# Kernel optimization log

Hardware: AMD Instinct MI355X
Metric: run time of the kernel (lower is better)

## Reference

```python
import jax, jax.numpy as jnp
import numpy as np

# Hamilton product tables: out component q uses weight IDX[q,p] with sign SGN[q,p]
# applied to input component p. Components order: (r, i, j, k); weights order: (rr, ri, rj, rk).
IDX = np.array([[0, 1, 2, 3], [1, 0, 3, 2], [2, 3, 0, 1], [3, 2, 1, 0]])
SGN = np.array([[1., -1., -1., -1.], [1., 1., 1., -1.], [1., -1., 1., 1.], [1., 1., -1., 1.]], dtype=np.float32)


def _qlinear(x4, w, b):
    # x4: (B, 4, Cin4, H, W); w: (4, Cout4, Cin4); b: (4, Cout4)
    # Quaternion 1x1 conv == channel-mixing matmul with Hamilton sign structure.
    wstk = jnp.asarray(SGN)[:, :, None, None] * w[IDX]  # (4,4,Cout4,Cin4)
    out = jnp.einsum('qpoc,bpchw->bqohw', wstk, x4)
    return out + b[None, :, :, None, None]


def _qdwconv(x4, w, b):
    # x4: (B, 4, Cc, H, W); w: (4, Cc, 1, 3, 3) depthwise per-channel; b: (4, Cc)
    Cc = x4.shape[2]
    comps = [x4[:, p] for p in range(4)]  # each (B, Cc, H, W)
    outs = []
    for qc in range(4):
        acc = None
        for p in range(4):
            c = SGN[qc, p] * jax.lax.conv_general_dilated(
                comps[p], w[IDX[qc, p]], window_strides=(1, 1), padding='SAME',
                feature_group_count=Cc, dimension_numbers=('NCHW', 'OIHW', 'NCHW'))
            acc = c if acc is None else acc + c
        outs.append(acc + b[qc][None, :, None, None])
    return jnp.stack(outs, axis=1)  # (B, 4, Cc, H, W)


def setup_inputs() -> dict:
    key = jax.random.key(0)
    ks = jax.random.split(key, 4)
    B, Cc, H, W = 8, 256, 32, 32   # dim = 4*Cc = 1024
    dim = 4 * Cc
    num_heads, key_dim = 8, 128
    h = 3 * num_heads * key_dim    # 3072 total -> 768 per component
    x = jax.random.normal(ks[0], (B, Cc, 4, H, W), jnp.float32)
    w_qkv = jax.random.normal(ks[1], (4, h // 4, dim // 4), jnp.float32) * (1.0 / np.sqrt(dim))
    b_qkv = jnp.zeros((4, h // 4), jnp.float32)
    w_proj = jax.random.normal(ks[2], (4, dim // 4, dim // 4), jnp.float32) * (1.0 / np.sqrt(dim))
    b_proj = jnp.zeros((4, dim // 4), jnp.float32)
    w_pe = jax.random.normal(ks[3], (4, dim // 4, 1, 3, 3), jnp.float32) * (1.0 / 6.0)
    b_pe = jnp.zeros((4, dim // 4), jnp.float32)
    return {'x': x, 'w_qkv': w_qkv, 'b_qkv': b_qkv, 'w_proj': w_proj,
            'b_proj': b_proj, 'w_pe': w_pe, 'b_pe': b_pe}


def reference(x, w_qkv, b_qkv, w_proj, b_proj, w_pe, b_pe):
    B, Cc, Q, H, W = x.shape
    num_heads, key_dim = 8, 128
    scale = key_dim ** -0.5
    N = H * W
    xq = jnp.transpose(x, (0, 2, 1, 3, 4))            # (B, 4, Cc, H, W)
    qkv = _qlinear(xq, w_qkv, b_qkv)                  # (B, 4, 768, H, W)
    q4, k4, v4 = jnp.split(qkv, 3, axis=2)            # each (B, 4, 256, H, W)

    def to_heads(t):  # (B,4,Cc,H,W) -> (B, heads, key_dim, N)
        return t.reshape(B, 4 * Cc, N).reshape(B, num_heads, key_dim, N)

    q, k, v = to_heads(q4), to_heads(k4), to_heads(v4)
    scores = jnp.einsum('bhdn,bhdm->bhnm', q, k) * scale   # (B,H,N,N) fully materialized
    attn = jax.nn.softmax(scores, axis=-1)
    out = jnp.einsum('bhnm,bhdm->bhdn', attn, v)           # (B,H,key_dim,N)
    out4 = out.reshape(B, 4, Cc, H, W)
    out = _qlinear(out4, w_proj, b_proj) + _qdwconv(xq, w_pe, b_pe)
    return jnp.transpose(out, (0, 2, 1, 3, 4))             # (B, Cc, 4, H, W)
```

## Files before the change

### kernel.cpp

```cpp
#include <hip/hip_runtime.h>
#include <hip/hip_bf16.h>

typedef unsigned short u16;
typedef float f32x4 __attribute__((ext_vector_type(4)));
typedef __bf16 bf16x8 __attribute__((ext_vector_type(8)));
typedef __bf16 bf16x4 __attribute__((ext_vector_type(4)));
typedef unsigned short su8v __attribute__((ext_vector_type(8)));
typedef unsigned short su4v __attribute__((ext_vector_type(4)));
typedef short s16x4 __attribute__((ext_vector_type(4)));

#define BB 8
#define NHD 8
#define DD 128
#define NN 1024
#define DIM 1024
#define H3 3072
#define MM 8192
#define QSC (0.08838834764831845f * 1.4426950408889634f)

__constant__ int   d_IDX[16] = {0,1,2,3, 1,0,3,2, 2,3,0,1, 3,2,1,0};
__constant__ float d_SGN[16] = {1.f,-1.f,-1.f,-1.f, 1.f,1.f,1.f,-1.f,
                                1.f,-1.f,1.f,1.f,  1.f,1.f,-1.f,1.f};

__device__ __forceinline__ f32x4 mfma16(su8v a, su8v b, f32x4 c) {
  return __builtin_amdgcn_mfma_f32_16x16x32_bf16(
      __builtin_bit_cast(bf16x8, a), __builtin_bit_cast(bf16x8, b), c, 0, 0, 0);
}
__device__ __forceinline__ f32x4 mfma16h(su4v a, su4v b, f32x4 c) {
#if __has_builtin(__builtin_amdgcn_mfma_f32_16x16x16_bf16)
  return __builtin_amdgcn_mfma_f32_16x16x16_bf16(
      __builtin_bit_cast(bf16x4, a), __builtin_bit_cast(bf16x4, b), c, 0, 0, 0);
#elif __has_builtin(__builtin_amdgcn_mfma_f32_16x16x16bf16_1k)
  return __builtin_amdgcn_mfma_f32_16x16x16bf16_1k(
      __builtin_bit_cast(s16x4, a), __builtin_bit_cast(s16x4, b), c, 0, 0, 0);
#else
  f32x4 d = c;
  asm("v_mfma_f32_16x16x16_bf16 %0, %1, %2, %0" : "+v"(d) : "v"(a), "v"(b));
  return d;
#endif
}
__device__ __forceinline__ u16 f2b(float f) {
  unsigned int u = __builtin_bit_cast(unsigned int, f);
  u += 0x7fffu + ((u >> 16) & 1u);
  return (u16)(u >> 16);
}
__device__ __forceinline__ float b2f(u16 v) {
  unsigned int u = ((unsigned int)v) << 16;
  return __builtin_bit_cast(float, u);
}
typedef const __attribute__((address_space(1))) unsigned int* gas_t;
typedef __attribute__((address_space(3))) unsigned int* las_t;
__device__ __forceinline__ void gll16(const u16* g, u16* l) {
  __builtin_amdgcn_global_load_lds((gas_t)g, (las_t)l, 16, 0, 0);
}

__global__ __launch_bounds__(256) void prep_weff(
    const float* __restrict__ wqkv, const float* __restrict__ wproj,
    u16* __restrict__ weffQ, u16* __restrict__ weffP) {
  int tid = blockIdx.x * 256 + threadIdx.x;
  int stride = gridDim.x * 256;
  for (int i = tid; i < H3 * DIM; i += stride) {
    int row = i >> 10, col = i & 1023;
    int q = row / 768, o = row - q * 768;
    int p = col >> 8, c = col & 255;
    float v = d_SGN[q * 4 + p] * wqkv[(d_IDX[q * 4 + p] * 768 + o) * 256 + c];
    if (o < 256) v *= QSC;
    weffQ[i] = f2b(v);
  }
  for (int i = tid; i < DIM * DIM; i += stride) {
    int row = i >> 10, col = i & 1023;
    int q = row >> 8, o = row & 255;
    int p = col >> 8, c = col & 255;
    weffP[i] = f2b(d_SGN[q * 4 + p] * wproj[(d_IDX[q * 4 + p] * 256 + o) * 256 + c]);
  }
}

__global__ __launch_bounds__(256) void prep_x(
    const float* __restrict__ x, u16* __restrict__ Ax) {
  __shared__ u16 T[64 * 264];
  int blk = blockIdx.x;
  int nc = blk & 15;
  int cc = (blk >> 4) & 3;
  int b = blk >> 6;
  int n0 = nc * 64, c0 = cc * 64;
  int tid = threadIdx.x;
  int nseg = tid & 15, rq = tid >> 4;
#pragma unroll
  for (int pass = 0; pass < 16; ++pass) {
    int rr = pass * 16 + rq;
    int p = rr >> 6, c = rr & 63;
    float4 f = *(const float4*)(x + (((size_t)(b * 256 + c0 + c)) * 4 + p) * 1024 +
                                n0 + nseg * 4);
    T[(nseg * 4 + 0) * 264 + rr] = f2b(f.x);
    T[(nseg * 4 + 1) * 264 + rr] = f2b(f.y);
    T[(nseg * 4 + 2) * 264 + rr] = f2b(f.z);
    T[(nseg * 4 + 3) * 264 + rr] = f2b(f.w);
  }
  __syncthreads();
  int nl = tid >> 5, lc = tid & 31;
#pragma unroll
  for (int pass = 0; pass < 8; ++pass) {
    int n = pass * 8 + nl;
    su8v v = *(const su8v*)(&T[n * 264 + lc * 8]);
    int pcl = lc * 8;
    *(su8v*)(Ax + (size_t)(b * 1024 + n0 + n) * 1024 + (pcl >> 6) * 256 + c0 +
             (pcl & 63)) = v;
  }
}

template <int BM, int BN>
__device__ __forceinline__ void gemm_core8(
    const u16* __restrict__ Ag, const u16* __restrict__ Bg,
    u16* As, u16* Bs, int tid, f32x4 (&acc)[4][4]) {
  constexpr int WN = BN / 64;
  constexpr int AC = BM / 64;
  constexpr int BC = BN / 64;
  constexpr int NT = 16;
  int w = tid >> 6, lane = tid & 63, l16 = lane & 15, quad = lane >> 4;
  int wm = w / WN, wn = w % WN;
  int x7 = l16 & 7;
  int srow = lane >> 3;
  int sblk = (lane & 7) ^ srow;

  auto STAGE_A = [&](int tt, int bs) {
#pragma unroll
    for (int c = 0; c < AC; ++c) {
      int r0 = c * 64 + w * 8;
      gll16(Ag + (size_t)(r0 + srow) * 1024 + tt * 64 + sblk * 8,
            As + (size_t)bs * (BM * 64) + r0 * 64);
    }
  };
  auto STAGE_B = [&](int tt, int bs) {
#pragma unroll
    for (int c = 0; c < BC; ++c) {
      int r0 = c * 64 + w * 8;
      gll16(Bg + (size_t)(r0 + srow) * 1024 + tt * 64 + sblk * 8,
            Bs + (size_t)bs * (BN * 64) + r0 * 64);
    }
  };

  STAGE_A(0, 0); STAGE_B(0, 0);
  STAGE_A(1, 1); STAGE_B(1, 1);
  asm volatile("s_waitcnt vmcnt(6)" ::: "memory");
  __builtin_amdgcn_s_barrier();

  int cur = 0, nxt = 1, stg = 2;
  for (int t = 0; t < NT; ++t) {
    const u16* At = As + (size_t)cur * (BM * 64);
    const u16* Bt = Bs + (size_t)cur * (BN * 64);
#pragma unroll
    for (int kk = 0; kk < 2; ++kk) {
      su8v af[4], bf[4];
#pragma unroll
      for (int i = 0; i < 4; ++i)
        af[i] = *(const su8v*)(At + (wm * 64 + i * 16 + l16) * 64 +
                               ((kk * 4 + quad) ^ x7) * 8);
#pragma unroll
      for (int j = 0; j < 4; ++j)
        bf[j] = *(const su8v*)(Bt + (wn * 64 + j * 16 + l16) * 64 +
                               ((kk * 4 + quad) ^ x7) * 8);
      if (t + 2 < NT) {
        if (kk == 0) STAGE_A(t + 2, stg);
        else         STAGE_B(t + 2, stg);
      }
      __builtin_amdgcn_s_setprio(1);
#pragma unroll
      for (int i = 0; i < 4; ++i)
#pragma unroll
        for (int j = 0; j < 4; ++j)
          acc[i][j] = mfma16(af[i], bf[j], acc[i][j]);
      __builtin_amdgcn_s_setprio(0);
    }
    if (t < NT - 2)       asm volatile("s_waitcnt vmcnt(6)" ::: "memory");
    else if (t == NT - 2) asm volatile("s_waitcnt vmcnt(0)" ::: "memory");
    asm volatile("" ::: "memory");
    __builtin_amdgcn_s_barrier();
    asm volatile("" ::: "memory");
    int tmp = cur; cur = nxt; nxt = stg; stg = tmp;
  }
}

__global__ __launch_bounds__(512, 2) void gemm_qkv_mfma(
    const u16* __restrict__ Ax, const u16* __restrict__ weffQ,
    const float* __restrict__ bqkv,
    u16* __restrict__ Qb, u16* __restrict__ Kb, u16* __restrict__ VbT) {
  __shared__ u16 smem[3 * 384 * 64];
  int bn0 = blockIdx.x * 256;
  int col0 = blockIdx.y * 128;
  int q = col0 / 768;
  int off = col0 - q * 768;
  int sel = off >> 8;
  int head = (q * 256 + (off & 255)) >> 7;
  int tid = threadIdx.x;
  int w = tid >> 6, lane = tid & 63, l16 = lane & 15, quad = lane >> 4;
  f32x4 acc[4][4];
#pragma unroll
  for (int i = 0; i < 4; ++i)
#pragma unroll
    for (int j = 0; j < 4; ++j) acc[i][j] = (f32x4){0.f, 0.f, 0.f, 0.f};

  if (sel == 2) {
    gemm_core8<256, 128>(Ax + (size_t)bn0 * 1024, weffQ + (size_t)col0 * 1024,
                         smem, smem + 3 * 256 * 64, tid, acc);
    int wm = w >> 1, wn = w & 1;
#pragma unroll
    for (int j = 0; j < 4; ++j) {
      int dl = wn * 64 + j * 16 + l16;
      float bias = bqkv[col0 + dl];
      int hswap = ((dl >> 3) & 1) << 2;
#pragma unroll
      for (int i = 0; i < 4; ++i) {
        int m = bn0 + wm * 64 + i * 16 + quad * 4;
        int b = m >> 10, npos = m & 1023;
        int bh = b * NHD + head;
        su4v pk;
#pragma unroll
        for (int r = 0; r < 4; ++r) pk[r] = f2b(acc[i][j][r] + bias);
        *(su4v*)(VbT + ((size_t)bh * DD + dl) * NN + (npos ^ hswap)) = pk;
      }
    }
  } else {
    gemm_core8<128, 256>(weffQ + (size_t)col0 * 1024, Ax + (size_t)bn0 * 1024,
                         smem, smem + 3 * 128 * 64, tid, acc);
    int wm = w >> 2, wn = w & 3;
    u16* dst = (sel == 0) ? Qb : Kb;
    float sc = (sel == 0) ? (float)QSC : 1.0f;
#pragma unroll
    for (int i = 0; i < 4; ++i) {
      int dbase = wm * 64 + i * 16 + quad * 4;
      float4 b4 = *(const float4*)(bqkv + col0 + dbase);
#pragma unroll
      for (int j = 0; j < 4; ++j) {
        int n = bn0 + wn * 64 + j * 16 + l16;
        int b = n >> 10, npos = n & 1023;
        int bh = b * NHD + head;
        su4v pk;
        pk[0] = f2b(acc[i][j][0] + b4.x * sc);
        pk[1] = f2b(acc[i][j][1] + b4.y * sc);
        pk[2] = f2b(acc[i][j][2] + b4.z * sc);
        pk[3] = f2b(acc[i][j][3] + b4.w * sc);
        *(su4v*)(dst + ((size_t)bh * NN + npos) * DD + dbase) = pk;
      }
    }
  }
}

__global__ __launch_bounds__(256) void attn_mfma(
    const u16* __restrict__ Qb, const u16* __restrict__ Kb,
    const u16* __restrict__ VbT, u16* __restrict__ OP,
    float* __restrict__ LS) {
  __shared__ u16 Ks[64 * 128];
  __shared__ u16 Vt[128 * 64];
  int blk = blockIdx.x;
  int bh = blk & 63;
  int rest = blk >> 6;
  int qt = rest & 7;
  int half = rest >> 3;
  int n0 = qt * 128;
  int tid = threadIdx.x;
  int w = tid >> 6, lane = tid & 63, l16 = lane & 15, quad = lane >> 4;
  const u16* Qg = Qb + ((size_t)bh * NN + n0) * DD;
  const u16* Kg = Kb + (size_t)bh * NN * DD;
  const u16* Vg = VbT + (size_t)bh * DD * NN;
  int x7 = l16 & 7;
  int vhalf = ((quad & 1) ^ (l16 >> 3)) * 4;

  su8v qreg[2][4];
#pragma unroll
  for (int mi = 0; mi < 2; ++mi)
#pragma unroll
    for (int ch = 0; ch < 4; ++ch)
      qreg[mi][ch] = *(const su8v*)(Qg + (size_t)(w * 32 + mi * 16 + l16) * DD +
                                    ch * 32 + quad * 8);

  su4v ones;
  ones[0] = 0x3F80; ones[1] = 0x3F80; ones[2] = 0x3F80; ones[3] = 0x3F80;
  f32x4 accL[2];
  accL[0] = (f32x4){0.f, 0.f, 0.f, 0.f};
  accL[1] = (f32x4){0.f, 0.f, 0.f, 0.f};
  f32x4 accO[2][8];
#pragma unroll
  for (int mi = 0; mi < 2; ++mi)
#pragma unroll
    for (int dt = 0; dt < 8; ++dt) accO[mi][dt] = (f32x4){0.f, 0.f, 0.f, 0.f};

  for (int kt = 0; kt < 8; ++kt) {
    int c0 = half * 512 + kt * 64;
    __syncthreads();
#pragma unroll
    for (int t = 0; t < 4; ++t) {
      int ci = w * 4 + t;
      int krow = ci * 4 + (lane >> 4);
      int kblk = (lane & 15) ^ (krow & 15);
      gll16(Kg + (size_t)(c0 + krow) * DD + kblk * 8, Ks + ci * 512);
      int dv = ci * 8 + (lane >> 3);
      int vblk = (lane & 7) ^ (dv & 7);
      gll16(Vg + (size_t)dv * NN + c0 + vblk * 8, Vt + ci * 512);
    }
    __syncthreads();

#pragma unroll
    for (int j = 0; j < 4; ++j) {
      f32x4 s0 = (f32x4){0.f, 0.f, 0.f, 0.f};
      f32x4 s1 = (f32x4){0.f, 0.f, 0.f, 0.f};
#pragma unroll
      for (int ch = 0; ch < 4; ++ch) {
        su8v kf = *(const su8v*)(Ks + (j * 16 + l16) * 128 +
                                 (((ch * 4 + quad) ^ l16) * 8));
        s0 = mfma16(kf, qreg[0][ch], s0);
        s1 = mfma16(kf, qreg[1][ch], s1);
      }
      su4v p0, p1;
#pragma unroll
      for (int r = 0; r < 4; ++r) {
        float pa = __builtin_exp2f(s0[r]);
        p0[r] = (u16)(__builtin_bit_cast(unsigned int, pa) >> 16);
        float pb = __builtin_exp2f(s1[r]);
        p1[r] = (u16)(__builtin_bit_cast(unsigned int, pb) >> 16);
      }
      accL[0] = mfma16h(p0, ones, accL[0]);
      accL[1] = mfma16h(p1, ones, accL[1]);
#pragma unroll
      for (int dt = 0; dt < 8; ++dt) {
        su4v vf = *(const su4v*)(Vt + (dt * 16 + l16) * 64 +
                                 ((((j * 2 + (quad >> 1)) ^ x7) << 3) + vhalf));
        accO[0][dt] = mfma16h(p0, vf, accO[0][dt]);
        accO[1][dt] = mfma16h(p1, vf, accO[1][dt]);
      }
    }
  }

  size_t hb = (size_t)(half * 64 + bh);
  if (l16 == 0) {
#pragma unroll
    for (int mi = 0; mi < 2; ++mi)
      *(float4*)(&LS[hb * NN + n0 + w * 32 + mi * 16 + quad * 4]) =
          *(float4*)(&accL[mi]);
  }
#pragma unroll
  for (int mi = 0; mi < 2; ++mi)
#pragma unroll
    for (int r = 0; r < 4; ++r) {
      int row = w * 32 + mi * 16 + quad * 4 + r;
      size_t base = (hb * NN + n0 + row) * DD;
#pragma unroll
      for (int dt = 0; dt < 8; ++dt)
        OP[base + dt * 16 + l16] = f2b(accO[mi][dt][r]);
    }
}

__global__ __launch_bounds__(256) void attn_merge(
    const u16* __restrict__ OP, const float* __restrict__ LS,
    u16* __restrict__ AO) {
  size_t idx = (size_t)blockIdx.x * 256 + threadIdx.x;
  size_t e = idx * 4;
  int d = (int)(e & 127);
  size_t bhn = e >> 7;
  su4v a = *(const su4v*)(OP + bhn * DD + d);
  su4v b = *(const su4v*)(OP + (size_t)64 * NN * DD + bhn * DD + d);
  float inv = 1.0f / (LS[bhn] + LS[bhn + 64 * NN]);
  int bh = (int)(bhn >> 10), n = (int)(bhn & 1023);
  int bb = bh >> 3, head = bh & 7;
  su4v o;
#pragma unroll
  for (int r = 0; r < 4; ++r) o[r] = f2b((b2f(a[r]) + b2f(b[r])) * inv);
  *(su4v*)(AO + ((size_t)(bb * 1024 + n) * 1024) + head * 128 + d) = o;
}

__global__ __launch_bounds__(256) void qdwconv_kernel(
    const float* __restrict__ x, const float* __restrict__ wpe,
    const float* __restrict__ bpe, float* __restrict__ pe) {
  int blk = blockIdx.x;
  int co = blk & 255;
  int b = blk >> 8;
  __shared__ float pl[4][34 * 34];
  __shared__ float wsm[4][9];
  int tid = threadIdx.x;
  for (int i = tid; i < 4 * 34 * 34; i += 256) ((float*)pl)[i] = 0.f;
  if (tid < 36) wsm[tid / 9][tid % 9] = wpe[((tid / 9) * 256 + co) * 9 + tid % 9];
  __syncthreads();
  for (int i = tid; i < 4 * 1024; i += 256) {
    int p = i >> 10, n = i & 1023;
    int h = n >> 5, ww = n & 31;
    pl[p][(h + 1) * 34 + (ww + 1)] =
        x[(((size_t)b * 256 + co) * 4 + p) * 1024 + n];
  }
  __syncthreads();
  for (int n = tid; n < 1024; n += 256) {
    int h = n >> 5, ww = n & 31;
    float in[4][9];
#pragma unroll
    for (int p = 0; p < 4; ++p)
#pragma unroll
      for (int t = 0; t < 9; ++t)
        in[p][t] = pl[p][(h + t / 3) * 34 + (ww + t % 3)];
#pragma unroll
    for (int q = 0; q < 4; ++q) {
      float acc = bpe[q * 256 + co];
#pragma unroll
      for (int p = 0; p < 4; ++p) {
        int idx = d_IDX[q * 4 + p];
        float s = d_SGN[q * 4 + p];
        float sub = 0.f;
#pragma unroll
        for (int t = 0; t < 9; ++t) sub += in[p][t] * wsm[idx][t];
        acc += s * sub;
      }
      pe[(((size_t)b * 256 + co) * 4 + q) * 1024 + n] = acc;
    }
  }
}

__global__ __launch_bounds__(512, 2) void gemm_proj_mfma(
    const u16* __restrict__ AO, const u16* __restrict__ weffP,
    const float* __restrict__ bproj, const float* __restrict__ pe,
    float* __restrict__ out) {
  __shared__ u16 smem[3 * 384 * 64];
  int n0 = blockIdx.x * 256;
  int m0 = blockIdx.y * 128;
  int tid = threadIdx.x;
  f32x4 acc[4][4];
#pragma unroll
  for (int i = 0; i < 4; ++i)
#pragma unroll
    for (int j = 0; j < 4; ++j) acc[i][j] = (f32x4){0.f, 0.f, 0.f, 0.f};
  gemm_core8<128, 256>(weffP + (size_t)m0 * 1024, AO + (size_t)n0 * 1024,
                       smem, smem + 3 * 128 * 64, tid, acc);

  int w = tid >> 6, lane = tid & 63, l16 = lane & 15, quad = lane >> 4;
  int wm = w >> 2, wn = w & 3;
#pragma unroll
  for (int i = 0; i < 4; ++i) {
#pragma unroll
    for (int r = 0; r < 4; ++r) {
      int mrow = m0 + wm * 64 + i * 16 + quad * 4 + r;
      int q = mrow >> 8, o = mrow & 255;
      float bias = bproj[mrow];
#pragma unroll
      for (int j = 0; j < 4; ++j) {
        int n = n0 + wn * 64 + j * 16 + l16;
        int b = n >> 10, npos = n & 1023;
        size_t oidx = (((size_t)b * 256 + o) * 4 + q) * 1024 + npos;
        out[oidx] = pe[oidx] + acc[i][j][r] + bias;
      }
    }
  }
}

extern "C" void kernel_launch(void* const* d_in, const int* in_sizes, int n_in,
                              void* d_out, int out_size, void* d_ws,
                              size_t ws_size, hipStream_t stream) {
  const float* x      = (const float*)d_in[0];
  const float* w_qkv  = (const float*)d_in[1];
  const float* b_qkv  = (const float*)d_in[2];
  const float* w_proj = (const float*)d_in[3];
  const float* b_proj = (const float*)d_in[4];
  const float* w_pe   = (const float*)d_in[5];
  const float* b_pe   = (const float*)d_in[6];
  float* out = (float*)d_out;

  u16* ws = (u16*)d_ws;
  u16* weffQ = ws;
  u16* weffP = weffQ + (size_t)H3 * DIM;
  u16* Ax    = weffP + (size_t)DIM * DIM;
  u16* Qb    = Ax + (size_t)MM * DIM;
  u16* Kb    = Qb + (size_t)BB * NHD * NN * DD;
  u16* VbT   = Kb + (size_t)BB * NHD * NN * DD;
  u16* AO    = VbT + (size_t)BB * NHD * DD * NN;
  float* PE  = (float*)(AO + (size_t)MM * DIM);
  u16* OP    = (u16*)(PE + (size_t)MM * DIM);
  float* LS  = (float*)(OP + (size_t)2 * 64 * NN * DD);

  hipLaunchKernelGGL(prep_weff, dim3(4096), dim3(256), 0, stream,
                     w_qkv, w_proj, weffQ, weffP);
  hipLaunchKernelGGL(prep_x, dim3(512), dim3(256), 0, stream, x, Ax);
  hipLaunchKernelGGL(gemm_qkv_mfma, dim3(MM / 256, H3 / 128), dim3(512), 0,
                     stream, Ax, weffQ, b_qkv, Qb, Kb, VbT);
  hipLaunchKernelGGL(attn_mfma, dim3(1024), dim3(256), 0, stream,
                     Qb, Kb, VbT, OP, LS);
  hipLaunchKernelGGL(attn_merge, dim3((64 * NN * DD) / (256 * 4)), dim3(256),
                     0, stream, OP, LS, AO);
  hipLaunchKernelGGL(qdwconv_kernel, dim3(BB * 256), dim3(256), 0, stream,
                     x, w_pe, b_pe, PE);
  hipLaunchKernelGGL(gemm_proj_mfma, dim3(MM / 256, DIM / 128), dim3(512), 0,
                     stream, AO, weffP, b_proj, PE, out);
}
```

Baseline: 290.1 us.

## Triple-buffer K/V tiles in attention with async prefetch and waitcnt pipelining

The attention kernel used to load a 64-key K/V tile, barrier, compute, then barrier again. It now uses 32-key tiles in a three-stage LDS ring and issues async loads two tiles ahead, with explicit vmcnt waits and a single barrier per iteration, so global loads overlap MFMA work. The V layout swizzle in the QKV writer and in the LDS reads is changed to fit the narrower tile. The trade-off is more iterations and barriers plus tighter waitcnt bookkeeping, which risks races if the counts are wrong.

Result: faster. 283.6 us (-2.2%).

```diff
diff --git a/kernel.cpp b/kernel.cpp
--- a/kernel.cpp
+++ b/kernel.cpp
@@ -207,7 +207,6 @@
     for (int j = 0; j < 4; ++j) {
       int dl = wn * 64 + j * 16 + l16;
       float bias = bqkv[col0 + dl];
-      int hswap = ((dl >> 3) & 1) << 2;
 #pragma unroll
       for (int i = 0; i < 4; ++i) {
         int m = bn0 + wm * 64 + i * 16 + quad * 4;
@@ -216,7 +215,7 @@
         su4v pk;
 #pragma unroll
         for (int r = 0; r < 4; ++r) pk[r] = f2b(acc[i][j][r] + bias);
-        *(su4v*)(VbT + ((size_t)bh * DD + dl) * NN + (npos ^ hswap)) = pk;
+        *(su4v*)(VbT + ((size_t)bh * DD + dl) * NN + npos) = pk;
       }
     }
   } else {
@@ -249,8 +248,8 @@
     const u16* __restrict__ Qb, const u16* __restrict__ Kb,
     const u16* __restrict__ VbT, u16* __restrict__ OP,
     float* __restrict__ LS) {
-  __shared__ u16 Ks[64 * 128];
-  __shared__ u16 Vt[128 * 64];
+  __shared__ u16 Ks[3 * 32 * 128];
+  __shared__ u16 Vt[3 * 128 * 32];
   int blk = blockIdx.x;
   int bh = blk & 63;
   int rest = blk >> 6;
@@ -262,8 +261,20 @@
   const u16* Qg = Qb + ((size_t)bh * NN + n0) * DD;
   const u16* Kg = Kb + (size_t)bh * NN * DD;
   const u16* Vg = VbT + (size_t)bh * DD * NN;
-  int x7 = l16 & 7;
-  int vhalf = ((quad & 1) ^ (l16 >> 3)) * 4;
+
+  auto STAGE = [&](int kt, int s) {
+    int c0 = half * 512 + kt * 32;
+#pragma unroll
+    for (int t = 0; t < 2; ++t) {
+      int ci = w * 2 + t;
+      int krow = ci * 4 + (lane >> 4);
+      int kblk = (lane & 15) ^ (krow & 15);
+      gll16(Kg + (size_t)(c0 + krow) * DD + kblk * 8, Ks + s * 4096 + ci * 512);
+      int dv = ci * 16 + (lane >> 2);
+      int vblk = (lane & 3) ^ ((dv >> 1) & 3);
+      gll16(Vg + (size_t)dv * NN + c0 + vblk * 8, Vt + s * 4096 + ci * 512);
+    }
+  };
 
   su8v qreg[2][4];
 #pragma unroll
@@ -284,28 +295,23 @@
 #pragma unroll
     for (int dt = 0; dt < 8; ++dt) accO[mi][dt] = (f32x4){0.f, 0.f, 0.f, 0.f};
 
-  for (int kt = 0; kt < 8; ++kt) {
-    int c0 = half * 512 + kt * 64;
-    __syncthreads();
-#pragma unroll
-    for (int t = 0; t < 4; ++t) {
-      int ci = w * 4 + t;
-      int krow = ci * 4 + (lane >> 4);
-      int kblk = (lane & 15) ^ (krow & 15);
-      gll16(Kg + (size_t)(c0 + krow) * DD + kblk * 8, Ks + ci * 512);
-      int dv = ci * 8 + (lane >> 3);
-      int vblk = (lane & 7) ^ (dv & 7);
-      gll16(Vg + (size_t)dv * NN + c0 + vblk * 8, Vt + ci * 512);
-    }
-    __syncthreads();
-
-#pragma unroll
-    for (int j = 0; j < 4; ++j) {
+  STAGE(0, 0); STAGE(1, 1);
+  asm volatile("s_waitcnt vmcnt(4)" ::: "memory");
+  __builtin_amdgcn_s_barrier();
+
+  int cur = 0, nxt = 1, stg = 2;
+  for (int kt = 0; kt < 16; ++kt) {
+    const u16* Kc = Ks + cur * 4096;
+    const u16* Vc = Vt + cur * 4096;
+    if (kt + 2 < 16) STAGE(kt + 2, stg);
+
+#pragma unroll
+    for (int j = 0; j < 2; ++j) {
       f32x4 s0 = (f32x4){0.f, 0.f, 0.f, 0.f};
       f32x4 s1 = (f32x4){0.f, 0.f, 0.f, 0.f};
 #pragma unroll
       for (int ch = 0; ch < 4; ++ch) {
-        su8v kf = *(const su8v*)(Ks + (j * 16 + l16) * 128 +
+        su8v kf = *(const su8v*)(Kc + (j * 16 + l16) * 128 +
                                  (((ch * 4 + quad) ^ l16) * 8));
         s0 = mfma16(kf, qreg[0][ch], s0);
         s1 = mfma16(kf, qreg[1][ch], s1);
@@ -322,12 +328,21 @@
       accL[1] = mfma16h(p1, ones, accL[1]);
 #pragma unroll
       for (int dt = 0; dt < 8; ++dt) {
-        su4v vf = *(const su4v*)(Vt + (dt * 16 + l16) * 64 +
-                                 ((((j * 2 + (quad >> 1)) ^ x7) << 3) + vhalf));
+        su4v vf = *(const su4v*)(Vc + (dt * 16 + l16) * 32 +
+                                 (((j * 4 + quad) ^ (l16 & 6)) * 4));
         accO[0][dt] = mfma16h(p0, vf, accO[0][dt]);
         accO[1][dt] = mfma16h(p1, vf, accO[1][dt]);
       }
     }
+
+    if (kt < 14)       asm volatile("s_waitcnt vmcnt(4)" ::: "memory");
+    else if (kt == 14) asm volatile("s_waitcnt vmcnt(0)" ::: "memory");
+    if (kt < 15) {
+      asm volatile("" ::: "memory");
+      __builtin_amdgcn_s_barrier();
+      asm volatile("" ::: "memory");
+    }
+    int tmp = cur; cur = nxt; nxt = stg; stg = tmp;
   }
 
   size_t hb = (size_t)(half * 64 + bh);
```
